# Optimization experiments

Hardware: AMD Instinct MI355X
Metric: run time of the kernel (lower is better)

Reference implementation:

```python
import jax, jax.numpy as jnp
import numpy as np

IN_F = 4096
OUT_F = 11008

def setup_inputs() -> dict:
    key = jax.random.key(0)
    k1, k2, k3, k4 = jax.random.split(key, 4)
    x = jax.random.normal(k1, (4, 128, IN_F), dtype=jnp.float32)
    # int8-style quantized weights stored as int32 in [-127, 127]
    quantized_weight = jax.random.randint(k2, (OUT_F, IN_F), -127, 128, dtype=jnp.int32)
    # per-output-row scale, kept away from zero
    scale = jax.random.uniform(k3, (OUT_F, 1), dtype=jnp.float32, minval=0.5, maxval=1.5)
    bias = jax.random.normal(k4, (OUT_F,), dtype=jnp.float32)
    return {"x": x, "quantized_weight": quantized_weight, "scale": scale, "bias": bias}

def reference(x, quantized_weight, scale, bias):
    # int8 dequantization: weight = q.float() / scale  -> [OUT_F, IN_F] fp32
    weight = quantized_weight.astype(jnp.float32) / scale
    # F.linear(x, weight, bias) == x @ weight.T + bias
    out = jnp.einsum('bsi,oi->bso', x, weight) + bias
    return out
```

## Files before the change

kernel.cpp:

```cpp
#include <hip/hip_runtime.h>
#include <hip/hip_bf16.h>
#include <stdint.h>

#define IN_F  4096
#define OUT_F 11008
#define MTOT  512

#define BM 128
#define BN 64
#define BK 64
#define NKT (IN_F / BK)
#define B_TILE_B (BN * BK * 2)
#define XT_B 16384
#define X_WS_BYTES ((size_t)MTOT * IN_F * 2)

typedef __attribute__((ext_vector_type(4))) float  f32x4;
typedef __attribute__((ext_vector_type(4))) int    i32x4;
typedef __attribute__((ext_vector_type(2))) unsigned u32x2;
typedef __attribute__((ext_vector_type(4))) unsigned u32x4;
typedef __attribute__((ext_vector_type(8))) __bf16 bf16x8;

__device__ __forceinline__ unsigned pack2bf16_rnd(float lo, float hi) {
    unsigned ulo = __builtin_bit_cast(unsigned, lo) + 0x8000u;
    unsigned uhi = __builtin_bit_cast(unsigned, hi) + 0x8000u;
    return __builtin_amdgcn_perm(uhi, ulo, 0x07060302u);
}
__device__ __forceinline__ unsigned pack2bf16_exact(float lo, float hi) {
    return __builtin_amdgcn_perm(__builtin_bit_cast(unsigned, hi),
                                 __builtin_bit_cast(unsigned, lo), 0x07060302u);
}

#define BAR() do {                                                 \
    asm volatile("s_waitcnt lgkmcnt(0)" ::: "memory");             \
    __builtin_amdgcn_s_barrier();                                  \
    __builtin_amdgcn_sched_barrier(0);                             \
} while (0)

__global__ __launch_bounds__(256)
void xconv_kernel(const float* __restrict__ X, char* __restrict__ xws) {
    const int gid  = blockIdx.x * 256 + threadIdx.x;
    const int row  = gid >> 9;
    const int col0 = (gid & 511) * 8;
    const float* src = X + (size_t)row * IN_F + col0;
    f32x4 v0 = *(const f32x4*)(src);
    f32x4 v1 = *(const f32x4*)(src + 4);
    u32x4 o;
    o.x = pack2bf16_rnd(v0.x, v0.y);
    o.y = pack2bf16_rnd(v0.z, v0.w);
    o.z = pack2bf16_rnd(v1.x, v1.y);
    o.w = pack2bf16_rnd(v1.z, v1.w);
    const int mtile = row >> 7, mrow = row & 127;
    const int mi = mrow >> 4,  l15 = mrow & 15;
    const int kt  = col0 >> 6;
    const int ks  = (col0 >> 5) & 1;
    const int lhi = (col0 >> 3) & 3;
    const int lane = lhi * 16 + l15;
    const int f = mi * 2 + ks;
    *(u32x4*)(xws + ((size_t)(mtile * NKT + kt) * 16 + f) * 1024
                  + lane * 16) = o;
}

__global__ __launch_bounds__(128, 2)
void qgemm_kernel(const char* __restrict__ xws,
                  const int*   __restrict__ W,
                  const float* __restrict__ scale,
                  const float* __restrict__ bias,
                  float* __restrict__ Out)
{
    __shared__ __align__(16) char smem[2 * B_TILE_B];
    char* bufB0 = smem;
    char* bufB1 = smem + B_TILE_B;

    const int tid  = (int)threadIdx.x;
    const int lane = tid & 63;
    const int w    = tid >> 6;

    const int bid = (int)blockIdx.x;
    const int xcd = bid & 7;
    const int j   = bid >> 3;
    const int mtile = (xcd & 1) * 2 + (j & 1);
    const int ntile = (xcd >> 1) * 43 + (j >> 1);
    const int brow = mtile * BM;
    const int bcol = ntile * BN;

    const int srow  = tid >> 4;
    const int scol4 = tid & 15;
    const int* Wp = W + (size_t)(bcol + srow) * IN_F + scol4 * 4;

    const char* xAw = xws + (size_t)mtile * (NKT * XT_B) + w * 8192 + lane * 16;

    i32x4 rb[8];
    bf16x8 afE[8], afO[8];
    f32x4 acc[4][4];
    #pragma unroll
    for (int i = 0; i < 4; ++i)
        #pragma unroll
        for (int jj = 0; jj < 4; ++jj)
            acc[i][jj] = (f32x4){0.f, 0.f, 0.f, 0.f};

    #define LOAD_A(AF, KT)                                                   \
        _Pragma("unroll")                                                    \
        for (int q = 0; q < 8; ++q)                                          \
            AF[q] = *(const bf16x8*)(xAw + (size_t)(KT) * XT_B + q * 1024);

    #define LOAD_B(KT)                                                       \
        _Pragma("unroll")                                                    \
        for (int k = 0; k < 8; ++k)                                          \
            rb[k] = *(const i32x4*)(Wp + (size_t)(KT) * BK                   \
                                       + (size_t)(k * 8) * IN_F);

    #define CONVERT_B(DSTB)                                                  \
        _Pragma("unroll")                                                    \
        for (int k = 0; k < 8; ++k) {                                        \
            const int row = srow + k * 8;                                    \
            const int off = (row * 128 + scol4 * 8) ^ ((row & 7) << 4);      \
            u32x2 bv;                                                        \
            bv.x = pack2bf16_exact((float)rb[k].x, (float)rb[k].y);          \
            bv.y = pack2bf16_exact((float)rb[k].z, (float)rb[k].w);          \
            *(u32x2*)((DSTB) + off) = bv;                                    \
        }

    #define MFMA_PHASE(AF, BUFB)                                             \
        _Pragma("unroll")                                                    \
        for (int ks = 0; ks < 2; ++ks) {                                     \
            bf16x8 bfr[4];                                                   \
            _Pragma("unroll")                                                \
            for (int ni = 0; ni < 4; ++ni) {                                 \
                const int row = ni * 16 + (lane & 15);                       \
                const int off = (row * 128 + ks * 64 + (lane >> 4) * 16)     \
                                ^ ((row & 7) << 4);                          \
                bfr[ni] = *(const bf16x8*)((BUFB) + off);                    \
            }                                                                \
            __builtin_amdgcn_s_setprio(1);                                   \
            _Pragma("unroll")                                                \
            for (int mi = 0; mi < 4; ++mi)                                   \
                _Pragma("unroll")                                            \
                for (int ni = 0; ni < 4; ++ni)                               \
                    acc[mi][ni] = __builtin_amdgcn_mfma_f32_16x16x32_bf16(   \
                        AF[mi * 2 + ks], bfr[ni], acc[mi][ni], 0, 0, 0);     \
            __builtin_amdgcn_s_setprio(0);                                   \
        }

    LOAD_B(0);
    CONVERT_B(bufB0);
    LOAD_A(afE, 0);
    LOAD_B(1);
    BAR();

    for (int kt2 = 0; kt2 < NKT; kt2 += 2) {
        const bool last = (kt2 == NKT - 2);

        LOAD_A(afO, kt2 + 1);
        CONVERT_B(bufB1);
        if (!last) LOAD_B(kt2 + 2);
        MFMA_PHASE(afE, bufB0);
        BAR();

        if (!last) {
            LOAD_A(afE, kt2 + 2);
            CONVERT_B(bufB0);
            LOAD_B(kt2 + 3);
        }
        MFMA_PHASE(afO, bufB1);
        if (!last) BAR();
    }

    #pragma unroll
    for (int ni = 0; ni < 4; ++ni) {
        const int col = bcol + ni * 16 + (lane & 15);
        const float inv = 1.0f / scale[col];
        const float bs  = bias[col];
        #pragma unroll
        for (int mi = 0; mi < 4; ++mi) {
            const int row0 = brow + w * 64 + mi * 16 + ((lane >> 4) << 2);
            #pragma unroll
            for (int jj = 0; jj < 4; ++jj)
                Out[(size_t)(row0 + jj) * OUT_F + col] = acc[mi][ni][jj] * inv + bs;
        }
    }

    #undef LOAD_A
    #undef LOAD_B
    #undef CONVERT_B
    #undef MFMA_PHASE
}

__global__ __launch_bounds__(128, 2)
void qgemm_fallback_kernel(const float* __restrict__ X,
                           const int*   __restrict__ W,
                           const float* __restrict__ scale,
                           const float* __restrict__ bias,
                           float* __restrict__ Out)
{
    __shared__ __align__(16) char smem[BM * BK * 2 + B_TILE_B];
    char* bufA = smem;
    char* bufB = smem + BM * BK * 2;

    const int tid  = (int)threadIdx.x;
    const int lane = tid & 63;
    const int w    = tid >> 6;

    const int bid  = (int)blockIdx.x;
    const int lbid = (bid & 7) * 86 + (bid >> 3);
    const int mtile = lbid & 3;
    const int ntile = lbid >> 2;
    const int brow = mtile * BM;
    const int bcol = ntile * BN;

    const int srow  = tid >> 4;
    const int scol4 = tid & 15;
    const int* Wp = W + (size_t)(bcol + srow) * IN_F + scol4 * 4;
    const float* Xp = X + (size_t)(brow + srow) * IN_F + scol4 * 4;

    f32x4 acc[4][4];
    #pragma unroll
    for (int i = 0; i < 4; ++i)
        #pragma unroll
        for (int jj = 0; jj < 4; ++jj)
            acc[i][jj] = (f32x4){0.f, 0.f, 0.f, 0.f};

    for (int kt = 0; kt < NKT; ++kt) {
        #pragma unroll
        for (int k = 0; k < 8; ++k) {
            i32x4 rb = *(const i32x4*)(Wp + (size_t)kt * BK + (size_t)(k * 8) * IN_F);
            const int row = srow + k * 8;
            const int off = (row * 128 + scol4 * 8) ^ ((row & 7) << 4);
            u32x2 bv;
            bv.x = pack2bf16_exact((float)rb.x, (float)rb.y);
            bv.y = pack2bf16_exact((float)rb.z, (float)rb.w);
            *(u32x2*)(bufB + off) = bv;
        }
        #pragma unroll
        for (int k = 0; k < 16; ++k) {
            f32x4 ra = *(const f32x4*)(Xp + (size_t)kt * BK + (size_t)(k * 8) * IN_F);
            const int row = srow + k * 8;
            const int off = (row * 128 + scol4 * 8) ^ ((row & 7) << 4);
            u32x2 av;
            av.x = pack2bf16_rnd(ra.x, ra.y);
            av.y = pack2bf16_rnd(ra.z, ra.w);
            *(u32x2*)(bufA + off) = av;
        }
        __syncthreads();
        #pragma unroll
        for (int ks = 0; ks < 2; ++ks) {
            bf16x8 af[4], bfr[4];
            #pragma unroll
            for (int mi = 0; mi < 4; ++mi) {
                const int row = w * 64 + mi * 16 + (lane & 15);
                const int off = (row * 128 + ks * 64 + (lane >> 4) * 16)
                                ^ ((row & 7) << 4);
                af[mi] = *(const bf16x8*)(bufA + off);
            }
            #pragma unroll
            for (int ni = 0; ni < 4; ++ni) {
                const int row = ni * 16 + (lane & 15);
                const int off = (row * 128 + ks * 64 + (lane >> 4) * 16)
                                ^ ((row & 7) << 4);
                bfr[ni] = *(const bf16x8*)(bufB + off);
            }
            #pragma unroll
            for (int mi = 0; mi < 4; ++mi)
                #pragma unroll
                for (int ni = 0; ni < 4; ++ni)
                    acc[mi][ni] = __builtin_amdgcn_mfma_f32_16x16x32_bf16(
                        af[mi], bfr[ni], acc[mi][ni], 0, 0, 0);
        }
        __syncthreads();
    }

    #pragma unroll
    for (int ni = 0; ni < 4; ++ni) {
        const int col = bcol + ni * 16 + (lane & 15);
        const float inv = 1.0f / scale[col];
        const float bs  = bias[col];
        #pragma unroll
        for (int mi = 0; mi < 4; ++mi) {
            const int row0 = brow + w * 64 + mi * 16 + ((lane >> 4) << 2);
            #pragma unroll
            for (int jj = 0; jj < 4; ++jj)
                Out[(size_t)(row0 + jj) * OUT_F + col] = acc[mi][ni][jj] * inv + bs;
        }
    }
}

extern "C" void kernel_launch(void* const* d_in, const int* in_sizes, int n_in,
                              void* d_out, int out_size, void* d_ws, size_t ws_size,
                              hipStream_t stream) {
    const float* X     = (const float*)d_in[0];
    const int*   W     = (const int*)d_in[1];
    const float* scale = (const float*)d_in[2];
    const float* bias  = (const float*)d_in[3];
    float* Out = (float*)d_out;

    const int grid = (MTOT / BM) * (OUT_F / BN);

    if (ws_size >= X_WS_BYTES) {
        char* xws = (char*)d_ws;
        xconv_kernel<<<(MTOT * IN_F / 8) / 256, 256, 0, stream>>>(X, xws);
        qgemm_kernel<<<grid, 128, 0, stream>>>(xws, W, scale, bias, Out);
    } else {
        qgemm_fallback_kernel<<<grid, 128, 0, stream>>>(X, W, scale, bias, Out);
    }
}
```

Measured before the change: 81.52 us.

## Quantize activations per-row to int8 and run an int8 MFMA GEMM on pre-packed weights

```diff
diff --git a/kernel.cpp b/kernel.cpp
--- a/kernel.cpp
+++ b/kernel.cpp
@@ -10,9 +10,16 @@
 #define BN 64
 #define BK 64
 #define NKT (IN_F / BK)
-#define B_TILE_B (BN * BK * 2)
-#define XT_B 16384
-#define X_WS_BYTES ((size_t)MTOT * IN_F * 2)
+#define NTILES (OUT_F / BN)
+
+#define XT_B 8192
+#define WT_B 4096
+
+#define SX_OFF   ((size_t)MTOT * IN_F)
+#define WWS_OFF  ((size_t)4 * 1024 * 1024)
+#define W_I8_BYTES ((size_t)NTILES * NKT * WT_B)
+#define WS_FULL  (WWS_OFF + W_I8_BYTES)
+#define WS_MID   ((size_t)MTOT * IN_F * 2)
 
 typedef __attribute__((ext_vector_type(4))) float  f32x4;
 typedef __attribute__((ext_vector_type(4))) int    i32x4;
@@ -29,6 +36,11 @@
     return __builtin_amdgcn_perm(__builtin_bit_cast(unsigned, hi),
                                  __builtin_bit_cast(unsigned, lo), 0x07060302u);
 }
+__device__ __forceinline__ unsigned pack4_i8(i32x4 v) {
+    unsigned r1 = __builtin_amdgcn_perm((unsigned)v.y, (unsigned)v.x, 0x00000400u);
+    unsigned r2 = __builtin_amdgcn_perm((unsigned)v.w, (unsigned)v.z, 0x00000400u);
+    return __builtin_amdgcn_perm(r2, r1, 0x05040100u);
+}
 
 #define BAR() do {                                                 \
     asm volatile("s_waitcnt lgkmcnt(0)" ::: "memory");             \
@@ -36,8 +48,166 @@
     __builtin_amdgcn_sched_barrier(0);                             \
 } while (0)
 
+
 __global__ __launch_bounds__(256)
-void xconv_kernel(const float* __restrict__ X, char* __restrict__ xws) {
+void xconv_i8_kernel(const float* __restrict__ X, char* __restrict__ xws,
+                     float* __restrict__ sx) {
+    const int row = (int)blockIdx.x;
+    const int t   = (int)threadIdx.x;
+    const float* src = X + (size_t)row * IN_F + t * 16;
+    f32x4 v0 = *(const f32x4*)(src);
+    f32x4 v1 = *(const f32x4*)(src + 4);
+    f32x4 v2 = *(const f32x4*)(src + 8);
+    f32x4 v3 = *(const f32x4*)(src + 12);
+
+    float m = 0.f;
+    #pragma unroll
+    for (int i = 0; i < 4; ++i)
+        m = fmaxf(m, fmaxf(fmaxf(fabsf(v0[i]), fabsf(v1[i])),
+                           fmaxf(fabsf(v2[i]), fabsf(v3[i]))));
+    #pragma unroll
+    for (int off = 32; off >= 1; off >>= 1)
+        m = fmaxf(m, __shfl_xor(m, off));
+    __shared__ float red[4];
+    if ((t & 63) == 0) red[t >> 6] = m;
+    __syncthreads();
+    m = fmaxf(fmaxf(red[0], red[1]), fmaxf(red[2], red[3]));
+    m = fmaxf(m, 1e-20f);
+    const float inv = 127.0f / m;
+    if (t == 0) sx[row] = m * (1.0f / 127.0f);
+
+    i32x4 q0, q1, q2, q3;
+    #pragma unroll
+    for (int i = 0; i < 4; ++i) {
+        q0[i] = (int)__builtin_rintf(v0[i] * inv);
+        q1[i] = (int)__builtin_rintf(v1[i] * inv);
+        q2[i] = (int)__builtin_rintf(v2[i] * inv);
+        q3[i] = (int)__builtin_rintf(v3[i] * inv);
+    }
+    u32x4 o;
+    o.x = pack4_i8(q0); o.y = pack4_i8(q1);
+    o.z = pack4_i8(q2); o.w = pack4_i8(q3);
+
+    const int mtile = row >> 7, mrow = row & 127;
+    const int f = mrow >> 4, l15 = mrow & 15;
+    const int kt = t >> 2;
+    const int h  = t & 3;
+    const int lane = h * 16 + l15;
+    *(u32x4*)(xws + ((size_t)(mtile * NKT + kt)) * XT_B + f * 1024
+                  + lane * 16) = o;
+}
+
+__global__ __launch_bounds__(256)
+void wconv_kernel(const int* __restrict__ W, char* __restrict__ wws) {
+    const int row = (int)blockIdx.x;
+    const int t   = (int)threadIdx.x;
+    const int* src = W + (size_t)row * IN_F + t * 16;
+    i32x4 a = *(const i32x4*)(src);
+    i32x4 b = *(const i32x4*)(src + 4);
+    i32x4 c = *(const i32x4*)(src + 8);
+    i32x4 d = *(const i32x4*)(src + 12);
+    u32x4 o;
+    o.x = pack4_i8(a); o.y = pack4_i8(b);
+    o.z = pack4_i8(c); o.w = pack4_i8(d);
+
+    const int ntile = row >> 6, nrow = row & 63;
+    const int f = nrow >> 4, l15 = nrow & 15;
+    const int kt = t >> 2;
+    const int h  = t & 3;
+    const int lane = h * 16 + l15;
+    *(u32x4*)(wws + ((size_t)(ntile * NKT + kt)) * WT_B + f * 1024
+                  + lane * 16) = o;
+}
+
+__global__ __launch_bounds__(128, 2)
+void qgemm_ff_kernel(const char* __restrict__ xi8, const float* __restrict__ sx,
+                     const char* __restrict__ wi8,
+                     const float* __restrict__ scale,
+                     const float* __restrict__ bias,
+                     float* __restrict__ Out)
+{
+    const int tid  = (int)threadIdx.x;
+    const int lane = tid & 63;
+    const int w    = tid >> 6;
+
+    const int bid  = (int)blockIdx.x;
+    const int lbid = (bid & 7) * 86 + (bid >> 3);
+    const int mtile = lbid & 3;
+    const int ntile = lbid >> 2;
+    const int brow = mtile * BM;
+    const int bcol = ntile * BN;
+
+    const char* xA = xi8 + (size_t)mtile * (NKT * XT_B) + (w * 4) * 1024
+                   + lane * 16;
+    const char* wB = wi8 + (size_t)ntile * (NKT * WT_B) + lane * 16;
+
+    i32x4 afE[4], afO[4], bfE[4], bfO[4];
+    i32x4 acc[4][4];
+    #pragma unroll
+    for (int i = 0; i < 4; ++i)
+        #pragma unroll
+        for (int jj = 0; jj < 4; ++jj)
+            acc[i][jj] = (i32x4){0, 0, 0, 0};
+
+    #define LOAD_AF(AF, KT)                                                  \
+        _Pragma("unroll")                                                    \
+        for (int mi = 0; mi < 4; ++mi)                                       \
+            AF[mi] = *(const i32x4*)(xA + (size_t)(KT) * XT_B + mi * 1024);
+
+    #define LOAD_BF(BF, KT)                                                  \
+        _Pragma("unroll")                                                    \
+        for (int ni = 0; ni < 4; ++ni)                                       \
+            BF[ni] = *(const i32x4*)(wB + (size_t)(KT) * WT_B + ni * 1024);
+
+    #define MFMA_FF(AF, BF)                                                  \
+        _Pragma("unroll")                                                    \
+        for (int mi = 0; mi < 4; ++mi)                                       \
+            _Pragma("unroll")                                                \
+            for (int ni = 0; ni < 4; ++ni)                                   \
+                acc[mi][ni] = __builtin_amdgcn_mfma_i32_16x16x64_i8(         \
+                    AF[mi], BF[ni], acc[mi][ni], 0, 0, 0);
+
+    LOAD_AF(afE, 0);
+    LOAD_BF(bfE, 0);
+
+    for (int kt2 = 0; kt2 < NKT; kt2 += 2) {
+        const bool more = (kt2 + 2 < NKT);
+        LOAD_AF(afO, kt2 + 1);
+        LOAD_BF(bfO, kt2 + 1);
+        MFMA_FF(afE, bfE);
+        if (more) {
+            LOAD_AF(afE, kt2 + 2);
+            LOAD_BF(bfE, kt2 + 2);
+        }
+        MFMA_FF(afO, bfO);
+    }
+
+    #pragma unroll
+    for (int ni = 0; ni < 4; ++ni) {
+        const int col = bcol + ni * 16 + (lane & 15);
+        const float inv = 1.0f / scale[col];
+        const float bs  = bias[col];
+        #pragma unroll
+        for (int mi = 0; mi < 4; ++mi) {
+            const int row0 = brow + w * 64 + mi * 16 + ((lane >> 4) << 2);
+            const f32x4 sxq = *(const f32x4*)(sx + row0);
+            #pragma unroll
+            for (int jj = 0; jj < 4; ++jj)
+                Out[(size_t)(row0 + jj) * OUT_F + col] =
+                    (float)acc[mi][ni][jj] * (sxq[jj] * inv) + bs;
+        }
+    }
+    #undef LOAD_AF
+    #undef LOAD_BF
+    #undef MFMA_FF
+}
+
+
+#define XT16_B 16384
+#define BT16_B (BN * BK * 2)
+
+__global__ __launch_bounds__(256)
+void xconv_bf16_kernel(const float* __restrict__ X, char* __restrict__ xws) {
     const int gid  = blockIdx.x * 256 + threadIdx.x;
     const int row  = gid >> 9;
     const int col0 = (gid & 511) * 8;
@@ -61,25 +231,24 @@
 }
 
 __global__ __launch_bounds__(128, 2)
-void qgemm_kernel(const char* __restrict__ xws,
-                  const int*   __restrict__ W,
-                  const float* __restrict__ scale,
-                  const float* __restrict__ bias,
-                  float* __restrict__ Out)
+void qgemm_bf16_kernel(const char* __restrict__ xws,
+                       const int*   __restrict__ W,
+                       const float* __restrict__ scale,
+                       const float* __restrict__ bias,
+                       float* __restrict__ Out)
 {
-    __shared__ __align__(16) char smem[2 * B_TILE_B];
+    __shared__ __align__(16) char smem[2 * BT16_B];
     char* bufB0 = smem;
-    char* bufB1 = smem + B_TILE_B;
+    char* bufB1 = smem + BT16_B;
 
     const int tid  = (int)threadIdx.x;
     const int lane = tid & 63;
     const int w    = tid >> 6;
 
-    const int bid = (int)blockIdx.x;
-    const int xcd = bid & 7;
-    const int j   = bid >> 3;
-    const int mtile = (xcd & 1) * 2 + (j & 1);
-    const int ntile = (xcd >> 1) * 43 + (j >> 1);
+    const int bid  = (int)blockIdx.x;
+    const int lbid = (bid & 7) * 86 + (bid >> 3);
+    const int mtile = lbid & 3;
+    const int ntile = lbid >> 2;
     const int brow = mtile * BM;
     const int bcol = ntile * BN;
 
@@ -87,7 +256,7 @@
     const int scol4 = tid & 15;
     const int* Wp = W + (size_t)(bcol + srow) * IN_F + scol4 * 4;
 
-    const char* xAw = xws + (size_t)mtile * (NKT * XT_B) + w * 8192 + lane * 16;
+    const char* xAw = xws + (size_t)mtile * (NKT * XT16_B) + w * 8192 + lane * 16;
 
     i32x4 rb[8];
     bf16x8 afE[8], afO[8];
@@ -98,18 +267,18 @@
         for (int jj = 0; jj < 4; ++jj)
             acc[i][jj] = (f32x4){0.f, 0.f, 0.f, 0.f};
 
-    #define LOAD_A(AF, KT)                                                   \
+    #define LOAD_A16(AF, KT)                                                 \
         _Pragma("unroll")                                                    \
         for (int q = 0; q < 8; ++q)                                          \
-            AF[q] = *(const bf16x8*)(xAw + (size_t)(KT) * XT_B + q * 1024);
-
-    #define LOAD_B(KT)                                                       \
+            AF[q] = *(const bf16x8*)(xAw + (size_t)(KT) * XT16_B + q * 1024);
+
+    #define LOAD_B16(KT)                                                     \
         _Pragma("unroll")                                                    \
         for (int k = 0; k < 8; ++k)                                          \
             rb[k] = *(const i32x4*)(Wp + (size_t)(KT) * BK                   \
                                        + (size_t)(k * 8) * IN_F);
 
-    #define CONVERT_B(DSTB)                                                  \
+    #define CONVERT_B16(DSTB)                                                \
         _Pragma("unroll")                                                    \
         for (int k = 0; k < 8; ++k) {                                        \
             const int row = srow + k * 8;                                    \
@@ -120,7 +289,7 @@
             *(u32x2*)((DSTB) + off) = bv;                                    \
         }
 
-    #define MFMA_PHASE(AF, BUFB)                                             \
+    #define MFMA16(AF, BUFB)                                                 \
         _Pragma("unroll")                                                    \
         for (int ks = 0; ks < 2; ++ks) {                                     \
             bf16x8 bfr[4];                                                   \
@@ -131,37 +300,33 @@
                                 ^ ((row & 7) << 4);                          \
                 bfr[ni] = *(const bf16x8*)((BUFB) + off);                    \
             }                                                                \
-            __builtin_amdgcn_s_setprio(1);                                   \
             _Pragma("unroll")                                                \
             for (int mi = 0; mi < 4; ++mi)                                   \
                 _Pragma("unroll")                                            \
                 for (int ni = 0; ni < 4; ++ni)                               \
                     acc[mi][ni] = __builtin_amdgcn_mfma_f32_16x16x32_bf16(   \
                         AF[mi * 2 + ks], bfr[ni], acc[mi][ni], 0, 0, 0);     \
-            __builtin_amdgcn_s_setprio(0);                                   \
-        }
-
-    LOAD_B(0);
-    CONVERT_B(bufB0);
-    LOAD_A(afE, 0);
-    LOAD_B(1);
+        }
+
+    LOAD_B16(0);
+    CONVERT_B16(bufB0);
+    LOAD_A16(afE, 0);
+    LOAD_B16(1);
     BAR();
 
     for (int kt2 = 0; kt2 < NKT; kt2 += 2) {
         const bool last = (kt2 == NKT - 2);
-
-        LOAD_A(afO, kt2 + 1);
-        CONVERT_B(bufB1);
-        if (!last) LOAD_B(kt2 + 2);
-        MFMA_PHASE(afE, bufB0);
+        LOAD_A16(afO, kt2 + 1);
+        CONVERT_B16(bufB1);
+        if (!last) LOAD_B16(kt2 + 2);
+        MFMA16(afE, bufB0);
         BAR();
-
         if (!last) {
-            LOAD_A(afE, kt2 + 2);
-            CONVERT_B(bufB0);
-            LOAD_B(kt2 + 3);
-        }
-        MFMA_PHASE(afO, bufB1);
+            LOAD_A16(afE, kt2 + 2);
+            CONVERT_B16(bufB0);
+            LOAD_B16(kt2 + 3);
+        }
+        MFMA16(afO, bufB1);
         if (!last) BAR();
     }
 
@@ -178,12 +343,12 @@
                 Out[(size_t)(row0 + jj) * OUT_F + col] = acc[mi][ni][jj] * inv + bs;
         }
     }
-
-    #undef LOAD_A
-    #undef LOAD_B
-    #undef CONVERT_B
-    #undef MFMA_PHASE
-}
+    #undef LOAD_A16
+    #undef LOAD_B16
+    #undef CONVERT_B16
+    #undef MFMA16
+}
+
 
 __global__ __launch_bounds__(128, 2)
 void qgemm_fallback_kernel(const float* __restrict__ X,
@@ -192,7 +357,7 @@
                            const float* __restrict__ bias,
                            float* __restrict__ Out)
 {
-    __shared__ __align__(16) char smem[BM * BK * 2 + B_TILE_B];
+    __shared__ __align__(16) char smem[BM * BK * 2 + BT16_B];
     char* bufA = smem;
     char* bufB = smem + BM * BK * 2;
 
@@ -294,10 +459,17 @@
 
     const int grid = (MTOT / BM) * (OUT_F / BN);
 
-    if (ws_size >= X_WS_BYTES) {
+    if (ws_size >= WS_FULL) {
+        char*  xi8 = (char*)d_ws;
+        float* sx  = (float*)((char*)d_ws + SX_OFF);
+        char*  wi8 = (char*)d_ws + WWS_OFF;
+        xconv_i8_kernel<<<MTOT, 256, 0, stream>>>(X, xi8, sx);
+        wconv_kernel<<<OUT_F, 256, 0, stream>>>(W, wi8);
+        qgemm_ff_kernel<<<grid, 128, 0, stream>>>(xi8, sx, wi8, scale, bias, Out);
+    } else if (ws_size >= WS_MID) {
         char* xws = (char*)d_ws;
-        xconv_kernel<<<(MTOT * IN_F / 8) / 256, 256, 0, stream>>>(X, xws);
-        qgemm_kernel<<<grid, 128, 0, stream>>>(xws, W, scale, bias, Out);
+        xconv_bf16_kernel<<<(MTOT * IN_F / 8) / 256, 256, 0, stream>>>(X, xws);
+        qgemm_bf16_kernel<<<grid, 128, 0, stream>>>(xws, W, scale, bias, Out);
     } else {
         qgemm_fallback_kernel<<<grid, 128, 0, stream>>>(X, W, scale, bias, Out);
     }
```

Measured after the change: 131.0 us. +60.7%, slower.
